# Kernel tuning notes

Measured on AMD Instinct MI355X. Metric: run time of the kernel, lower is better.

Reference implementation:

```python
import jax, jax.numpy as jnp
import numpy as np

EPS = 1e-6
NEG = 0.2  # leaky-relu negative slope
OBJ_C = 6

def _knn(x, k):
    # x: [B,3,N] -> [B,N,k] indices of k nearest neighbors (incl. self)
    xx = jnp.sum(x * x, axis=1)
    inner = jnp.einsum('bdn,bdm->bnm', x, x)
    pd = 2.0 * inner - xx[:, :, None] - xx[:, None, :]  # negative sq dist
    return jax.lax.top_k(pd, k)[1]

def _gather_pts(xt, idx):
    # xt [B,N,D], idx [B,N,k] -> [B,N,k,D]
    return xt[jnp.arange(xt.shape[0])[:, None, None], idx]

def _vn_lin(W, x):
    # channel-mixing linear over VN channel dim: x [B,Cin,3,...]
    return jnp.einsum('oc,bc...->bo...', W, x)

def _vn_bn(x, g, b, eps=1e-5):
    # VNBatchNorm with batch statistics on vector norms
    n = jnp.linalg.norm(x, axis=2) + EPS          # [B,C,*spatial]
    axes = (0,) + tuple(range(2, n.ndim))
    m = jnp.mean(n, axes, keepdims=True)
    v = jnp.var(n, axes, keepdims=True)
    shp = (1, -1) + (1,) * (n.ndim - 2)
    nb = g.reshape(shp) * (n - m) / jnp.sqrt(v + eps) + b.reshape(shp)
    return x / n[:, :, None] * nb[:, :, None]

def _vn_leaky(p, d):
    dot = jnp.sum(p * d, axis=2, keepdims=True)
    dsq = jnp.sum(d * d, axis=2, keepdims=True)
    return NEG * p + (1.0 - NEG) * jnp.where(dot >= 0, p, p - (dot / (dsq + EPS)) * d)

def _vn_block(x, wf, wd, g=None, b=None):
    # VNLinearLeakyReLU
    p = _vn_lin(wf, x)
    if g is not None:
        p = _vn_bn(p, g, b)
    return _vn_leaky(p, _vn_lin(wd, x))

def _surface_feature(coord, k):
    # coord [B,3,N] -> [B,3(chan),3(vec),N,k]: (nb-ctr, ctr, nb x ctr)
    idx = _knn(coord, k)
    xt = coord.transpose(0, 2, 1)                                  # [B,N,3]
    nb = _gather_pts(xt, idx)[:, :, :, None, :]                    # [B,N,k,1,3]
    ctr = jnp.broadcast_to(xt[:, :, None, None, :], nb.shape)
    f = jnp.concatenate([nb - ctr, ctr, jnp.cross(nb, ctr, axis=-1)], axis=3)
    return f.transpose(0, 3, 4, 1, 2)

def _neighbor_feature(x, coord, k):
    # x [B,C,3,N], knn over coord -> [B,C,3,N,k]
    B, C, _, N = x.shape
    idx = _knn(coord, k)
    xt = x.reshape(B, C * 3, N).transpose(0, 2, 1)                 # [B,N,C*3]
    f = _gather_pts(xt, idx).reshape(B, N, k, C, 3)
    return f.transpose(0, 3, 4, 1, 2)

def _vn_maxpool_down(x, coord, wd, rate):
    # x [B,C,3,N,k]: stride-subsample points, VN-max over k neighbors
    x = x[:, :, :, ::rate, :]
    coord_d = coord[:, :, ::rate]
    dot = jnp.sum(x * _vn_lin(wd, x), axis=2)                      # [B,C,Nd,k]
    idx = jnp.argmax(dot, axis=-1)
    xm = jnp.take_along_axis(x, idx[:, :, None, :, None], axis=-1)[..., 0]
    return xm, coord_d

def _nearest_index(t, s):
    # t [B,N,3], s [B,M,3] -> argmin sq-dist index [B,N]
    d = jnp.sum(t * t, -1)[:, :, None] - 2.0 * jnp.einsum('bnd,bmd->bnm', t, s) + jnp.sum(s * s, -1)[:, None, :]
    return jnp.argmin(d, axis=-1)

def _index_points(x, idx):
    # x [B,C,3,M], idx [B,N] -> [B,C,3,N]
    xt = x.transpose(0, 3, 1, 2)
    return xt[jnp.arange(x.shape[0])[:, None], idx].transpose(0, 2, 3, 1)

def _conv_bn_relu(x, w, b, g, be, eps=1e-5):
    # 1x1 Conv1d + BatchNorm1d (batch stats) + ReLU
    y = jnp.einsum('oc,bcn->bon', w, x) + b[None, :, None]
    m = jnp.mean(y, (0, 2), keepdims=True)
    v = jnp.var(y, (0, 2), keepdims=True)
    return jax.nn.relu(g[None, :, None] * (y - m) / jnp.sqrt(v + eps) + be[None, :, None])

def _forward(x, norm, cat_id, wf0, wd0, g0, b0, wf1, wd1, g1, b1, wp1, wf2, wd2, g2, b2, wf3, wd3, g3, b3, wp2, wf4, wd4, g4, b4, wv1f, wv1d, wv2f, wv2d, w3, ws1, cb1, sg1, sb1, ws2, cb2, sg2, sb2, ws3, cb3, sg3, sb3):
    B, _, _, N = x.shape
    coord = x.reshape(B, 3, N)
    one_hot = jax.nn.one_hot(cat_id, OBJ_C, dtype=x.dtype)
    x0 = _vn_block(_surface_feature(coord, 20), wf0, wd0, g0, b0).mean(-1)   # [B,42,3,N]
    x1 = _vn_block(x0, wf1, wd1, g1, b1)
    x2, coord2 = _vn_maxpool_down(_neighbor_feature(x1, coord, 4), coord, wp1, 4)
    x2 = _vn_block(x2, wf2, wd2, g2, b2)                                     # [B,84,3,N/4]
    x3 = _vn_block(x2, wf3, wd3, g3, b3)
    x4, coord4 = _vn_maxpool_down(_neighbor_feature(x3, coord2, 4), coord2, wp2, 4)
    x4 = _vn_block(x4, wf4, wd4, g4, b4)                                     # [B,168,3,N/16]
    ct = coord.transpose(0, 2, 1)
    i1 = _nearest_index(ct, coord2.transpose(0, 2, 1))
    i2 = _nearest_index(ct, coord4.transpose(0, 2, 1))
    eqv = jnp.concatenate([x0, x1, _index_points(x2, i1), _index_points(x3, i1), _index_points(x4, i2)], axis=1)  # [B,420,3,N]
    mean_feat = eqv.mean(-1, keepdims=True)                                  # [B,420,3,1]
    z = _vn_block(mean_feat, wv1f, wv1d)
    z = _vn_block(z, wv2f, wv2d)
    z = jnp.einsum('bcvm,kc->bvkm', z, w3)                                   # [B,3,2,1]
    inv_gl = jnp.einsum('bijm,bjkm->bikm', mean_feat, z).reshape(B, -1, 1)   # [B,840,1]
    inv_0 = jnp.broadcast_to(inv_gl, (B, inv_gl.shape[1], N))
    inv_1 = jnp.sum(mean_feat * coord[:, None], axis=2)                      # [B,420,N]
    oh = jnp.broadcast_to(one_hot[:, :, None], (B, OBJ_C, N))
    inv = jnp.concatenate([norm, inv_0, inv_1, oh], axis=1)                  # [B,1267,N]
    inv = _conv_bn_relu(inv, ws1, cb1, sg1, sb1)
    inv = _conv_bn_relu(inv, ws2, cb2, sg2, sb2)
    inv = _conv_bn_relu(inv, ws3, cb3, sg3, sb3)                             # [B,420,N]
    return eqv, mean_feat, inv, inv_gl

def setup_inputs():
    key = jax.random.key(0)
    ki = iter(jax.random.split(key, 40))
    B, N, D = 4, 2048, 42
    def lin(o, c):
        return jax.random.normal(next(ki), (o, c), jnp.float32) / float(np.sqrt(c))
    inp = dict(
        x=jax.random.normal(next(ki), (B, 1, 3, N), jnp.float32),
        norm=jax.random.normal(next(ki), (B, 1, N), jnp.float32),
        cat_id=jax.random.randint(next(ki), (B,), 0, OBJ_C),
        wf0=lin(D, 3), wd0=lin(D, 3), g0=jnp.ones(D), b0=jnp.zeros(D),
        wf1=lin(D, D), wd1=lin(D, D), g1=jnp.ones(D), b1=jnp.zeros(D),
        wp1=lin(D, D),
        wf2=lin(2 * D, D), wd2=lin(2 * D, D), g2=jnp.ones(2 * D), b2=jnp.zeros(2 * D),
        wf3=lin(2 * D, 2 * D), wd3=lin(2 * D, 2 * D), g3=jnp.ones(2 * D), b3=jnp.zeros(2 * D),
        wp2=lin(2 * D, 2 * D),
        wf4=lin(4 * D, 2 * D), wd4=lin(4 * D, 2 * D), g4=jnp.ones(4 * D), b4=jnp.zeros(4 * D),
        wv1f=lin(5 * D, 10 * D), wv1d=lin(5 * D, 10 * D),
        wv2f=lin(2 * D, 5 * D), wv2d=lin(2 * D, 5 * D),
        w3=lin(2, 2 * D),
        ws1=lin(1024, 1267), cb1=jnp.zeros(1024), sg1=jnp.ones(1024), sb1=jnp.zeros(1024),
        ws2=lin(512, 1024), cb2=jnp.zeros(512), sg2=jnp.ones(512), sb2=jnp.zeros(512),
        ws3=lin(420, 512), cb3=jnp.zeros(420), sg3=jnp.ones(420), sb3=jnp.zeros(420),
    )
    return inp

def reference(x, norm, cat_id, wf0, wd0, g0, b0, wf1, wd1, g1, b1, wp1, wf2, wd2, g2, b2, wf3, wd3, g3, b3, wp2, wf4, wd4, g4, b4, wv1f, wv1d, wv2f, wv2d, w3, ws1, cb1, sg1, sb1, ws2, cb2, sg2, sb2, ws3, cb3, sg3, sb3):
    return _forward(x, norm, cat_id, wf0, wd0, g0, b0, wf1, wd1, g1, b1, wp1, wf2, wd2, g2, b2, wf3, wd3, g3, b3, wp2, wf4, wd4, g4, b4, wv1f, wv1d, wv2f, wv2d, w3, ws1, cb1, sg1, sb1, ws2, cb2, sg2, sb2, ws3, cb3, sg3, sb3)
```

## Files before the change

### kernel.cpp

```cpp
#include <hip/hip_runtime.h>
#include <hip/hip_bf16.h>
#include <cstdint>
#include <cstddef>

#define NTOT 2048
#define BTOT 4

typedef short bf16x8 __attribute__((ext_vector_type(8)));
typedef float f32x4 __attribute__((ext_vector_type(4)));

__device__ inline unsigned short f2b(float v) {
    __hip_bfloat16 h = __float2bfloat16(v);
    return *reinterpret_cast<unsigned short*>(&h);
}

static const size_t WS_IDX20 = 0;
static const size_t WS_FS    = 163840;
static const size_t WS_X0    = 1638400;
static const size_t WS_X1    = 3702784;
static const size_t WS_XM2   = 5767168;
static const size_t WS_X2    = 6025216;
static const size_t WS_X3    = 6541312;
static const size_t WS_IDX42 = 7057408;
static const size_t WS_XM4   = 7059456;
static const size_t WS_X4    = 7188480;
static const size_t WS_I1    = 7446528;
static const size_t WS_I2    = 7454720;
static const size_t WS_MF    = 7462912;
static const size_t WS_INVGL = 7467952;
static const size_t WS_STATS = 7471312;
static const size_t WS_CST   = 7472992;
static const size_t WS_CB    = 7480320;
static const size_t WS_AB    = 7484416;
static const size_t WS_W0    = 7496704;
static const size_t WS_Z1    = 7497728;
static const size_t WS_Z2    = 7500288;
static const size_t WS_W2B   = 13378560;
static const size_t WS_W3B   = 13640704;
static const size_t WS_Y1T   = 13771776;
static const size_t WS_Y1B   = 0;
static const size_t WS_Y2T   = 7480320;
static const size_t WS_Y2B   = 4194304;
static const size_t WS_Y3T   = WS_Y1T;

#define ST0_OFF 0
#define ST1_OFF 84
#define ST2_OFF 168
#define ST3_OFF 336
#define ST4_OFF 504
#define CST1_OFF 0
#define CST2_OFF 2048
#define CST3_OFF 3072

#define OUT_EQV   0
#define OUT_MF    10321920
#define OUT_INV   10326960
#define OUT_INVGL 13767600

__device__ __forceinline__ void merge_pair(float& v1, int& m1, float& v2, int& m2,
                                           float w1, int n1, float w2, int n2)
{
    bool g  = (w1 > v1) || (w1 == v1 && n1 < m1);
    bool ga = (v1 > w2) || (v1 == w2 && m1 < n2);
    bool gb = (w1 > v2) || (w1 == v2 && n1 < m2);
    float s2v = g ? (ga ? v1 : w2) : (gb ? w1 : v2);
    int   s2m = g ? (ga ? m1 : n2) : (gb ? n1 : m2);
    float s1v = g ? w1 : v1;
    int   s1m = g ? n1 : m1;
    v1 = s1v; m1 = s1m; v2 = s2v; m2 = s2m;
}

__device__ __forceinline__ void qtop2(const float* v, int base,
                                      float& a1, int& j1, float& a2, int& j2)
{
    a1 = v[base]; j1 = base; a2 = -3.4e38f; j2 = base;
#pragma unroll
    for (int j = 1; j < 8; ++j) {
        float val = v[base + j];
        bool b1 = val > a1;
        bool b2 = val > a2;
        float na2 = b1 ? a1 : (b2 ? val : a2);
        int   nj2 = b1 ? j1 : (b2 ? base + j : j2);
        a1 = b1 ? val : a1;
        j1 = b1 ? base + j : j1;
        a2 = na2; j2 = nj2;
    }
}

template <int SLOTS, int K>
__global__ __launch_bounds__(256)
void knn_reg_kernel(const float* __restrict__ coord, int cand_stride, int q_stride,
                    int* __restrict__ out_idx, int q_cnt)
{
#pragma clang fp contract(off)
    constexpr int Q = SLOTS / 8;
    int b = blockIdx.y;
    int wave = threadIdx.x >> 6, lane = threadIdx.x & 63;
    int q = blockIdx.x * 4 + wave;
    if (q >= q_cnt) return;
    int nq = q * q_stride;
    float qx = coord[(b * 3 + 0) * NTOT + nq];
    float qy = coord[(b * 3 + 1) * NTOT + nq];
    float qz = coord[(b * 3 + 2) * NTOT + nq];
    float xxq = qx * qx + qy * qy + qz * qz;
    float v[SLOTS];
#pragma unroll
    for (int j = 0; j < SLOTS; ++j) {
        int mo = (lane + 64 * j) * cand_stride;
        float cx = coord[(b * 3 + 0) * NTOT + mo];
        float cy = coord[(b * 3 + 1) * NTOT + mo];
        float cz = coord[(b * 3 + 2) * NTOT + mo];
        float inner = qx * cx + qy * cy + qz * cz;
        float xxc = cx * cx + cy * cy + cz * cz;
        v[j] = (2.0f * inner - xxq) - xxc;
    }
    float q1v[Q], q2v[Q]; int q1j[Q], q2j[Q];
#pragma unroll
    for (int qq = 0; qq < Q; ++qq)
        qtop2(v, qq * 8, q1v[qq], q1j[qq], q2v[qq], q2j[qq]);

#pragma clang loop unroll(disable)
    for (int r = 0; r < K / 2; ++r) {
        float b1v, b2v; int b1j, b2j;
        if constexpr (Q == 4) {
            float x1v = q1v[0], x2v = q2v[0]; int x1j = q1j[0], x2j = q2j[0];
            merge_pair(x1v, x1j, x2v, x2j, q1v[1], q1j[1], q2v[1], q2j[1]);
            float y1v = q1v[2], y2v = q2v[2]; int y1j = q1j[2], y2j = q2j[2];
            merge_pair(y1v, y1j, y2v, y2j, q1v[3], q1j[3], q2v[3], q2j[3]);
            merge_pair(x1v, x1j, x2v, x2j, y1v, y1j, y2v, y2j);
            b1v = x1v; b1j = x1j; b2v = x2v; b2j = x2j;
        } else {
            b1v = q1v[0]; b1j = q1j[0]; b2v = q2v[0]; b2j = q2j[0];
        }
        int b1m = lane + (b1j << 6);
        int b2m = lane + (b2j << 6);
        for (int off = 32; off; off >>= 1) {
            float o1v = __shfl_xor(b1v, off); int o1m = __shfl_xor(b1m, off);
            float o2v = __shfl_xor(b2v, off); int o2m = __shfl_xor(b2m, off);
            merge_pair(b1v, b1m, b2v, b2m, o1v, o1m, o2v, o2m);
        }
        if (lane == 0) {
            out_idx[((size_t)(b * q_cnt) + q) * K + 2 * r]     = b1m;
            out_idx[((size_t)(b * q_cnt) + q) * K + 2 * r + 1] = b2m;
        }
        if (r == K / 2 - 1) break;
        int ws1 = __builtin_amdgcn_readfirstlane(b1m);
        int ws2 = __builtin_amdgcn_readfirstlane(b2m);
        int sl1 = ws1 >> 6, sl2 = ws2 >> 6;
        int wl1 = ws1 & 63, wl2 = ws2 & 63;
#pragma unroll
        for (int qq = 0; qq < Q; ++qq) {
            if ((sl1 >> 3) == qq || (sl2 >> 3) == qq) {
#pragma unroll
                for (int j = 0; j < 8; ++j) {
                    int sl = qq * 8 + j;
                    if (sl == sl1) v[sl] = (lane == wl1) ? -3.4e38f : v[sl];
                    if (sl == sl2) v[sl] = (lane == wl2) ? -3.4e38f : v[sl];
                }
                qtop2(v, qq * 8, q1v[qq], q1j[qq], q2v[qq], q2j[qq]);
            }
        }
    }
}

template <int SLOTS>
__global__ __launch_bounds__(256)
void nearest_reg_kernel(const float* __restrict__ coord, int cand_stride,
                        int* __restrict__ out)
{
#pragma clang fp contract(off)
    int b = blockIdx.y;
    int wave = threadIdx.x >> 6, lane = threadIdx.x & 63;
    int n = blockIdx.x * 4 + wave;
    float qx = coord[(b * 3 + 0) * NTOT + n];
    float qy = coord[(b * 3 + 1) * NTOT + n];
    float qz = coord[(b * 3 + 2) * NTOT + n];
    float tt = qx * qx + qy * qy + qz * qz;
    float v[SLOTS];
#pragma unroll
    for (int j = 0; j < SLOTS; ++j) {
        int mo = (lane + 64 * j) * cand_stride;
        float cx = coord[(b * 3 + 0) * NTOT + mo];
        float cy = coord[(b * 3 + 1) * NTOT + mo];
        float cz = coord[(b * 3 + 2) * NTOT + mo];
        float inner = qx * cx + qy * cy + qz * cz;
        float ss = cx * cx + cy * cy + cz * cz;
        v[j] = (tt - 2.0f * inner) + ss;
    }
    float bv = v[0];
    int bj = 0;
#pragma unroll
    for (int j = 1; j < SLOTS; ++j)
        if (v[j] < bv) { bv = v[j]; bj = j; }
    int bm = lane + 64 * bj;
    for (int off = 32; off; off >>= 1) {
        float ov = __shfl_down(bv, off);
        int   om = __shfl_down(bm, off);
        if (ov < bv || (ov == bv && om < bm)) { bv = ov; bm = om; }
    }
    if (lane == 0) out[b * NTOT + n] = bm;
}

__global__ __launch_bounds__(256)
void stats0_kernel(const float* __restrict__ coord, const int* __restrict__ idx20,
                   const float* __restrict__ wf0, double* __restrict__ stats)
{
    __shared__ float nbc[360];
    __shared__ float ctr[18];
    __shared__ double red[2][6][42];
    int t = threadIdx.x, b = blockIdx.y;
    int ps = t / 42, o = t - ps * 42;
    bool active = ps < 6;
    float w0 = 0.f, w1 = 0.f, w2 = 0.f;
    if (active) { w0 = wf0[o * 3]; w1 = wf0[o * 3 + 1]; w2 = wf0[o * 3 + 2]; }
    double s = 0.0, s2 = 0.0;
    int base = blockIdx.x * 48;
    for (int it = 0; it < 8; ++it) {
        int n0 = base + it * 6;
        __syncthreads();
        if (t < 120) {
            int pl = t / 20, k = t - pl * 20;
            int n = n0 + pl; if (n > NTOT - 1) n = NTOT - 1;
            int m = idx20[((size_t)(b * NTOT + n)) * 20 + k];
            nbc[t * 3 + 0] = coord[(b * 3 + 0) * NTOT + m];
            nbc[t * 3 + 1] = coord[(b * 3 + 1) * NTOT + m];
            nbc[t * 3 + 2] = coord[(b * 3 + 2) * NTOT + m];
        }
        if (t >= 128 && t < 146) {
            int i = t - 128; int pl = i / 3, vd = i - pl * 3;
            int n = n0 + pl; if (n > NTOT - 1) n = NTOT - 1;
            ctr[i] = coord[(b * 3 + vd) * NTOT + n];
        }
        __syncthreads();
        if (active && n0 + ps < NTOT) {
            float cx = ctr[ps * 3], cy = ctr[ps * 3 + 1], cz = ctr[ps * 3 + 2];
            const float* nb = &nbc[ps * 60];
            for (int k = 0; k < 20; ++k) {
                float nx = nb[k * 3], ny = nb[k * 3 + 1], nz = nb[k * 3 + 2];
                float dx = nx - cx, dy = ny - cy, dz = nz - cz;
                float crx = ny * cz - nz * cy;
                float cry = nz * cx - nx * cz;
                float crz = nx * cy - ny * cx;
                float p0 = w0 * dx + w1 * cx + w2 * crx;
                float p1 = w0 * dy + w1 * cy + w2 * cry;
                float p2 = w0 * dz + w1 * cz + w2 * crz;
                float nrm = sqrtf(p0 * p0 + p1 * p1 + p2 * p2) + 1e-6f;
                s += (double)nrm; s2 += (double)nrm * (double)nrm;
            }
        }
    }
    if (active) { red[0][ps][o] = s; red[1][ps][o] = s2; }
    __syncthreads();
    if (t < 42) {
        double a = 0.0, a2 = 0.0;
#pragma unroll
        for (int p = 0; p < 6; ++p) { a += red[0][p][t]; a2 += red[1][p][t]; }
        atomicAdd(&stats[t], a);
        atomicAdd(&stats[42 + t], a2);
    }
}

__global__ __launch_bounds__(256)
void apply0_kernel(const float* __restrict__ coord, const int* __restrict__ idx20,
                   const float* __restrict__ wf0, const float* __restrict__ wd0,
                   const float* __restrict__ g0, const float* __restrict__ b0,
                   const double* __restrict__ stats, float* __restrict__ x0)
{
    __shared__ float nbc[360];
    __shared__ float ctr[18];
    int t = threadIdx.x;
    int b = blockIdx.y;
    int ps = t / 42, o = t - ps * 42;
    int n0 = blockIdx.x * 6;
    if (t < 120) {
        int pl = t / 20, k = t - pl * 20;
        int n = n0 + pl; if (n > NTOT - 1) n = NTOT - 1;
        int m = idx20[((size_t)(b * NTOT + n)) * 20 + k];
        nbc[t * 3 + 0] = coord[(b * 3 + 0) * NTOT + m];
        nbc[t * 3 + 1] = coord[(b * 3 + 1) * NTOT + m];
        nbc[t * 3 + 2] = coord[(b * 3 + 2) * NTOT + m];
    }
    if (t >= 128 && t < 146) {
        int i = t - 128; int pl = i / 3, vd = i - pl * 3;
        int n = n0 + pl; if (n > NTOT - 1) n = NTOT - 1;
        ctr[i] = coord[(b * 3 + vd) * NTOT + n];
    }
    __syncthreads();
    int n = n0 + ps;
    if (ps >= 6 || n >= NTOT) return;
    double S1 = stats[o], S2 = stats[42 + o];
    double md = S1 / 163840.0;
    float m = (float)md;
    float var = (float)(S2 / 163840.0 - md * md);
    float gs = g0[o] / sqrtf(var + 1e-5f);
    float bb = b0[o];
    float wa0 = wf0[o * 3], wa1 = wf0[o * 3 + 1], wa2 = wf0[o * 3 + 2];
    float wb0 = wd0[o * 3], wb1 = wd0[o * 3 + 1], wb2 = wd0[o * 3 + 2];
    float cx = ctr[ps * 3], cy = ctr[ps * 3 + 1], cz = ctr[ps * 3 + 2];
    const float* nb = &nbc[ps * 60];
    float a0 = 0.f, a1 = 0.f, a2 = 0.f;
    for (int k = 0; k < 20; ++k) {
        float nx = nb[k * 3], ny = nb[k * 3 + 1], nz = nb[k * 3 + 2];
        float dx = nx - cx, dy = ny - cy, dz = nz - cz;
        float crx = ny * cz - nz * cy;
        float cry = nz * cx - nx * cz;
        float crz = nx * cy - ny * cx;
        float p0 = wa0 * dx + wa1 * cx + wa2 * crx;
        float p1 = wa0 * dy + wa1 * cy + wa2 * cry;
        float p2 = wa0 * dz + wa1 * cz + wa2 * crz;
        float d0 = wb0 * dx + wb1 * cx + wb2 * crx;
        float d1 = wb0 * dy + wb1 * cy + wb2 * cry;
        float d2 = wb0 * dz + wb1 * cz + wb2 * crz;
        float nrm = sqrtf(p0 * p0 + p1 * p1 + p2 * p2) + 1e-6f;
        float nbv = gs * (nrm - m) + bb;
        float sc = nbv / nrm;
        p0 *= sc; p1 *= sc; p2 *= sc;
        float dot = p0 * d0 + p1 * d1 + p2 * d2;
        float dsq = d0 * d0 + d1 * d1 + d2 * d2 + 1e-6f;
        float tq = fminf(dot, 0.f) / dsq;
        a0 += 0.2f * p0 + 0.8f * (p0 - tq * d0);
        a1 += 0.2f * p1 + 0.8f * (p1 - tq * d1);
        a2 += 0.2f * p2 + 0.8f * (p2 - tq * d2);
    }
    x0[((size_t)(b * 42 + o) * 3 + 0) * NTOT + n] = a0 / 20.0f;
    x0[((size_t)(b * 42 + o) * 3 + 1) * NTOT + n] = a1 / 20.0f;
    x0[((size_t)(b * 42 + o) * 3 + 2) * NTOT + n] = a2 / 20.0f;
}

template <int Ci, int Co, int PTS, int NT, int NIT>
__global__ __launch_bounds__(NT)
void vn_stats_kernel(const float* __restrict__ xin,
                     const float* __restrict__ wf,
                     double* __restrict__ stats, int Npts)
{
    constexpr int Ci3 = Ci * 3;
    constexpr int STRIDE = Ci3 + 1;
    __shared__ float col[PTS * STRIDE];
    __shared__ double red[2][PTS][Co];
    int t = threadIdx.x;
    int b = blockIdx.y;
    int ps = t / Co;
    int o = t - ps * Co;
    bool active = ps < PTS;
    double s = 0.0, s2 = 0.0;
    int base = blockIdx.x * (PTS * NIT);
    for (int it = 0; it < NIT; ++it) {
        int pt0 = base + it * PTS;
        __syncthreads();
        for (int i = t; i < PTS * Ci3; i += NT) {
            int pl = i / Ci3, off = i - pl * Ci3;
            int pt = pt0 + pl; if (pt >= Npts) pt = Npts - 1;
            col[pl * STRIDE + off] = xin[(size_t)(b * 3 * Ci + off) * Npts + pt];
        }
        __syncthreads();
        if (active && pt0 + ps < Npts) {
            const float* cl = &col[ps * STRIDE];
            const float* wr = wf + o * Ci;
            float p0 = 0.f, p1 = 0.f, p2 = 0.f;
#pragma unroll
            for (int c = 0; c < Ci; ++c) {
                float w = wr[c];
                p0 += w * cl[3 * c]; p1 += w * cl[3 * c + 1]; p2 += w * cl[3 * c + 2];
            }
            float nrm = sqrtf(p0 * p0 + p1 * p1 + p2 * p2) + 1e-6f;
            s += (double)nrm; s2 += (double)nrm * (double)nrm;
        }
    }
    if (active) { red[0][ps][o] = s; red[1][ps][o] = s2; }
    __syncthreads();
    if (t < Co) {
        double a = 0.0, a2 = 0.0;
#pragma unroll
        for (int p = 0; p < PTS; ++p) { a += red[0][p][t]; a2 += red[1][p][t]; }
        atomicAdd(&stats[t], a);
        atomicAdd(&stats[Co + t], a2);
    }
}

template <int Ci, int Co, int PTS, int NT>
__global__ __launch_bounds__(NT)
void vn_apply_kernel(const float* __restrict__ xin,
                     const float* __restrict__ wf,
                     const float* __restrict__ wd,
                     const float* __restrict__ g,
                     const float* __restrict__ bbp,
                     const double* __restrict__ stats,
                     double count, int Npts,
                     float* __restrict__ xout)
{
    constexpr int Ci3 = Ci * 3;
    constexpr int STRIDE = Ci3 + 1;
    __shared__ float col[PTS * STRIDE];
    int t = threadIdx.x;
    int b = blockIdx.y;
    int ps = t / Co;
    int o = t - ps * Co;
    bool active = ps < PTS;
    float m = 0.f, gs = 0.f, bb = 0.f;
    if (active) {
        double S1 = stats[o], S2 = stats[Co + o];
        double md = S1 / count;
        m = (float)md;
        float var = (float)(S2 / count - md * md);
        gs = g[o] / sqrtf(var + 1e-5f);
        bb = bbp[o];
    }
    int pt0 = blockIdx.x * PTS;
    for (int i = t; i < PTS * Ci3; i += NT) {
        int pl = i / Ci3, off = i - pl * Ci3;
        int pt = pt0 + pl; if (pt >= Npts) pt = Npts - 1;
        col[pl * STRIDE + off] = xin[(size_t)(b * 3 * Ci + off) * Npts + pt];
    }
    __syncthreads();
    int pt = pt0 + ps;
    if (!active || pt >= Npts) return;
    const float* cl = &col[ps * STRIDE];
    const float* wr = wf + o * Ci;
    const float* wdr = wd + o * Ci;
    float p0 = 0.f, p1 = 0.f, p2 = 0.f, d0 = 0.f, d1 = 0.f, d2 = 0.f;
#pragma unroll
    for (int c = 0; c < Ci; ++c) {
        float c0 = cl[3 * c], c1 = cl[3 * c + 1], c2 = cl[3 * c + 2];
        float w = wr[c];
        p0 += w * c0; p1 += w * c1; p2 += w * c2;
        float w2 = wdr[c];
        d0 += w2 * c0; d1 += w2 * c1; d2 += w2 * c2;
    }
    float nrm = sqrtf(p0 * p0 + p1 * p1 + p2 * p2) + 1e-6f;
    float nb = gs * (nrm - m) + bb;
    float sc = nb / nrm;
    p0 *= sc; p1 *= sc; p2 *= sc;
    float dot = p0 * d0 + p1 * d1 + p2 * d2;
    float dsq = d0 * d0 + d1 * d1 + d2 * d2 + 1e-6f;
    float tq = fminf(dot, 0.f) / dsq;
    float r0 = p0 - tq * d0, r1 = p1 - tq * d1, r2 = p2 - tq * d2;
    xout[((size_t)(b * Co + o) * 3 + 0) * Npts + pt] = 0.2f * p0 + 0.8f * r0;
    xout[((size_t)(b * Co + o) * 3 + 1) * Npts + pt] = 0.2f * p1 + 0.8f * r1;
    xout[((size_t)(b * Co + o) * 3 + 2) * Npts + pt] = 0.2f * p2 + 0.8f * r2;
}

__global__ void vn_pool_kernel(const float* __restrict__ xin,
                               const int* __restrict__ idx, long long sb, int sq,
                               const float* __restrict__ wp,
                               float* __restrict__ xout,
                               int C, int Np, int Nq)
{
#pragma clang fp contract(off)
    __shared__ float nb[4 * 84 * 3];
    int b = blockIdx.y;
    int q = blockIdx.x;
    const int* ir = idx + b * sb + (long long)q * sq;
    for (int kk = 0; kk < 4; ++kk) {
        int mm = ir[kk];
        for (int t = threadIdx.x; t < C * 3; t += blockDim.x)
            nb[kk * C * 3 + t] = xin[(size_t)(b * 3 * C + t) * Np + mm];
    }
    __syncthreads();
    int o = threadIdx.x;
    if (o >= C) return;
    const float* wr = wp + o * C;
    float best = -3.4e38f;
    int bk = 0;
    for (int kk = 0; kk < 4; ++kk) {
        const float* cl = &nb[kk * C * 3];
        float d0 = 0.f, d1 = 0.f, d2 = 0.f;
        for (int c = 0; c < C; ++c) {
            float w = wr[c];
            d0 += w * cl[3 * c]; d1 += w * cl[3 * c + 1]; d2 += w * cl[3 * c + 2];
        }
        float dot = cl[o * 3] * d0 + cl[o * 3 + 1] * d1 + cl[o * 3 + 2] * d2;
        if (dot > best) { best = dot; bk = kk; }
    }
    const float* cb = &nb[bk * C * 3];
    xout[((size_t)(b * C + o) * 3 + 0) * Nq + q] = cb[o * 3];
    xout[((size_t)(b * C + o) * 3 + 1) * Nq + q] = cb[o * 3 + 1];
    xout[((size_t)(b * C + o) * 3 + 2) * Nq + q] = cb[o * 3 + 2];
}

__global__ void eqv_kernel(const float* __restrict__ x0, const float* __restrict__ x1,
                           const float* __restrict__ x2, const float* __restrict__ x3,
                           const float* __restrict__ x4,
                           const int* __restrict__ i1, const int* __restrict__ i2,
                           float* __restrict__ out_eqv, float* __restrict__ mfw)
{
    __shared__ float r1[256];
    int n = blockIdx.x * 256 + threadIdx.x;
    int cv = blockIdx.y;
    int b = blockIdx.z;
    int cc = cv / 3, v = cv % 3;
    float val;
    if (cc < 42)
        val = x0[((size_t)(b * 42 + cc) * 3 + v) * NTOT + n];
    else if (cc < 84)
        val = x1[((size_t)(b * 42 + (cc - 42)) * 3 + v) * NTOT + n];
    else if (cc < 168) {
        int m = i1[b * NTOT + n];
        val = x2[((size_t)(b * 84 + (cc - 84)) * 3 + v) * 512 + m];
    } else if (cc < 252) {
        int m = i1[b * NTOT + n];
        val = x3[((size_t)(b * 84 + (cc - 168)) * 3 + v) * 512 + m];
    } else {
        int m = i2[b * NTOT + n];
        val = x4[((size_t)(b * 168 + (cc - 252)) * 3 + v) * 128 + m];
    }
    out_eqv[((size_t)(b * 1260 + cv)) * NTOT + n] = val;
    r1[threadIdx.x] = val;
    __syncthreads();
    for (int off = 128; off; off >>= 1) {
        if ((int)threadIdx.x < off) r1[threadIdx.x] += r1[threadIdx.x + off];
        __syncthreads();
    }
    if (threadIdx.x == 0) atomicAdd(&mfw[b * 1260 + cv], r1[0]);
}

__global__ void mf_finalize_kernel(float* __restrict__ mfw, float* __restrict__ out_mf)
{
    int i = blockIdx.x * 256 + threadIdx.x;
    if (i < 5040) {
        float m = mfw[i] / 2048.0f;
        mfw[i] = m;
        out_mf[i] = m;
    }
}

__global__ __launch_bounds__(256)
void z1_kernel(const float* __restrict__ mfw,
               const float* __restrict__ wv1f, const float* __restrict__ wv1d,
               float* __restrict__ z1ws)
{
    __shared__ float mf[1260];
    int b = blockIdx.y;
    int wave = threadIdx.x >> 6, lane = threadIdx.x & 63;
    for (int i = threadIdx.x; i < 1260; i += 256) mf[i] = mfw[b * 1260 + i];
    __syncthreads();
    int o = blockIdx.x * 4 + wave;
    if (o >= 210) return;
    const float* wr  = wv1f + (size_t)o * 420;
    const float* wdr = wv1d + (size_t)o * 420;
    float p0 = 0.f, p1 = 0.f, p2 = 0.f, d0 = 0.f, d1 = 0.f, d2 = 0.f;
    for (int c = lane; c < 420; c += 64) {
        float m0 = mf[3 * c], m1 = mf[3 * c + 1], m2 = mf[3 * c + 2];
        float w = wr[c];
        p0 += w * m0; p1 += w * m1; p2 += w * m2;
        float w2 = wdr[c];
        d0 += w2 * m0; d1 += w2 * m1; d2 += w2 * m2;
    }
    for (int off = 32; off; off >>= 1) {
        p0 += __shfl_down(p0, off); p1 += __shfl_down(p1, off);
        p2 += __shfl_down(p2, off); d0 += __shfl_down(d0, off);
        d1 += __shfl_down(d1, off); d2 += __shfl_down(d2, off);
    }
    if (lane == 0) {
        float dot = p0 * d0 + p1 * d1 + p2 * d2;
        float r0, r1, r2;
        if (dot >= 0.f) { r0 = p0; r1 = p1; r2 = p2; }
        else {
            float tq = dot / (d0 * d0 + d1 * d1 + d2 * d2 + 1e-6f);
            r0 = p0 - tq * d0; r1 = p1 - tq * d1; r2 = p2 - tq * d2;
        }
        z1ws[b * 630 + o * 3]     = 0.2f * p0 + 0.8f * r0;
        z1ws[b * 630 + o * 3 + 1] = 0.2f * p1 + 0.8f * r1;
        z1ws[b * 630 + o * 3 + 2] = 0.2f * p2 + 0.8f * r2;
    }
}

__global__ __launch_bounds__(256)
void z2_kernel(const float* __restrict__ z1ws,
               const float* __restrict__ wv2f, const float* __restrict__ wv2d,
               float* __restrict__ z2ws)
{
    __shared__ float zl[630];
    int b = blockIdx.y;
    int wave = threadIdx.x >> 6, lane = threadIdx.x & 63;
    for (int i = threadIdx.x; i < 630; i += 256) zl[i] = z1ws[b * 630 + i];
    __syncthreads();
    int o = blockIdx.x * 4 + wave;
    if (o >= 84) return;
    const float* wr  = wv2f + (size_t)o * 210;
    const float* wdr = wv2d + (size_t)o * 210;
    float p0 = 0.f, p1 = 0.f, p2 = 0.f, d0 = 0.f, d1 = 0.f, d2 = 0.f;
    for (int c = lane; c < 210; c += 64) {
        float m0 = zl[3 * c], m1 = zl[3 * c + 1], m2 = zl[3 * c + 2];
        float w = wr[c];
        p0 += w * m0; p1 += w * m1; p2 += w * m2;
        float w2 = wdr[c];
        d0 += w2 * m0; d1 += w2 * m1; d2 += w2 * m2;
    }
    for (int off = 32; off; off >>= 1) {
        p0 += __shfl_down(p0, off); p1 += __shfl_down(p1, off);
        p2 += __shfl_down(p2, off); d0 += __shfl_down(d0, off);
        d1 += __shfl_down(d1, off); d2 += __shfl_down(d2, off);
    }
    if (lane == 0) {
        float dot = p0 * d0 + p1 * d1 + p2 * d2;
        float r0, r1, r2;
        if (dot >= 0.f) { r0 = p0; r1 = p1; r2 = p2; }
        else {
            float tq = dot / (d0 * d0 + d1 * d1 + d2 * d2 + 1e-6f);
            r0 = p0 - tq * d0; r1 = p1 - tq * d1; r2 = p2 - tq * d2;
        }
        z2ws[b * 252 + o * 3]     = 0.2f * p0 + 0.8f * r0;
        z2ws[b * 252 + o * 3 + 1] = 0.2f * p1 + 0.8f * r1;
        z2ws[b * 252 + o * 3 + 2] = 0.2f * p2 + 0.8f * r2;
    }
}

__global__ void z3invgl_kernel(const float* __restrict__ mfw,
                               const float* __restrict__ z2ws,
                               const float* __restrict__ w3,
                               float* __restrict__ invgl_ws,
                               float* __restrict__ out_invgl)
{
    __shared__ float z2[252];
    __shared__ float z3[6];
    __shared__ float mf[1260];
    int b = blockIdx.x;
    int t = threadIdx.x;
    for (int i = t; i < 252; i += 256) z2[i] = z2ws[b * 252 + i];
    for (int i = t; i < 1260; i += 256) mf[i] = mfw[b * 1260 + i];
    __syncthreads();
    if (t < 6) {
        int v = t / 2, kt = t % 2;
        float s = 0.f;
        for (int c = 0; c < 84; ++c) s += z2[c * 3 + v] * w3[kt * 84 + c];
        z3[v * 2 + kt] = s;
    }
    __syncthreads();
    for (int i = t; i < 840; i += 256) {
        int ii = i / 2, kt = i % 2;
        float s = mf[ii * 3] * z3[0 + kt] + mf[ii * 3 + 1] * z3[2 + kt] +
                  mf[ii * 3 + 2] * z3[4 + kt];
        invgl_ws[b * 840 + i] = s;
        out_invgl[b * 840 + i] = s;
    }
}

__global__ __launch_bounds__(256)
void conv1_coef_kernel(const float* __restrict__ ws1,
                       const float* __restrict__ invgl,
                       const float* __restrict__ mfw,
                       const int* __restrict__ cat,
                       float* __restrict__ cb, float* __restrict__ ab,
                       float* __restrict__ w0)
{
    int wave = threadIdx.x >> 6, lane = threadIdx.x & 63;
    int o = blockIdx.x * 4 + wave;
    int b = blockIdx.y;
    const float* wr = ws1 + (size_t)o * 1267;
    float s = 0.f;
    for (int j = lane; j < 840; j += 64)
        s += wr[1 + j] * invgl[b * 840 + j];
    float a0 = 0.f, a1 = 0.f, a2 = 0.f;
    for (int i = lane; i < 420; i += 64) {
        float w = wr[841 + i];
        a0 += w * mfw[b * 1260 + i * 3];
        a1 += w * mfw[b * 1260 + i * 3 + 1];
        a2 += w * mfw[b * 1260 + i * 3 + 2];
    }
    for (int off = 32; off; off >>= 1) {
        s  += __shfl_down(s, off);
        a0 += __shfl_down(a0, off);
        a1 += __shfl_down(a1, off);
        a2 += __shfl_down(a2, off);
    }
    if (lane == 0) {
        cb[b * 1024 + o] = s + wr[1261 + cat[b]];
        ab[((size_t)(b * 1024 + o)) * 3 + 0] = a0;
        ab[((size_t)(b * 1024 + o)) * 3 + 1] = a1;
        ab[((size_t)(b * 1024 + o)) * 3 + 2] = a2;
        if (b == 0) w0[o] = wr[0];
    }
}

__global__ __launch_bounds__(256)
void y1_stats_kernel(const float* __restrict__ cb, const float* __restrict__ ab,
                     const float* __restrict__ w0, const float* __restrict__ coord,
                     const float* __restrict__ normv, float* __restrict__ cst)
{
    __shared__ float px[256], py[256], pz[256], pn[256];
    int t = threadIdx.x;
    int o = blockIdx.x * 256 + t;
    int b = blockIdx.y >> 3;
    int n0 = (blockIdx.y & 7) * 256;
    px[t] = coord[(b * 3 + 0) * NTOT + n0 + t];
    py[t] = coord[(b * 3 + 1) * NTOT + n0 + t];
    pz[t] = coord[(b * 3 + 2) * NTOT + n0 + t];
    pn[t] = normv[b * NTOT + n0 + t];
    __syncthreads();
    size_t bo = (size_t)(b * 1024 + o);
    float c0 = cb[bo];
    float a0 = ab[bo * 3], a1 = ab[bo * 3 + 1], a2 = ab[bo * 3 + 2];
    float wn = w0[o];
    float s = 0.f, s2 = 0.f;
    for (int k = 0; k < 256; ++k) {
        float v = c0 + a0 * px[k] + a1 * py[k] + a2 * pz[k] + wn * pn[k];
        s += v; s2 += v * v;
    }
    atomicAdd(&cst[o], s);
    atomicAdd(&cst[1024 + o], s2);
}

__global__ __launch_bounds__(256)
void y1_bnrelu_kernel(const float* __restrict__ cb, const float* __restrict__ ab,
                      const float* __restrict__ w0, const float* __restrict__ coord,
                      const float* __restrict__ normv, const float* __restrict__ cst,
                      const float* __restrict__ sg, const float* __restrict__ sb,
                      unsigned short* __restrict__ y1b)
{
    __shared__ float px[256], py[256], pz[256], pn[256];
    int t = threadIdx.x;
    int o = blockIdx.x * 256 + t;
    int b = blockIdx.y >> 3;
    int n0 = (blockIdx.y & 7) * 256;
    px[t] = coord[(b * 3 + 0) * NTOT + n0 + t];
    py[t] = coord[(b * 3 + 1) * NTOT + n0 + t];
    pz[t] = coord[(b * 3 + 2) * NTOT + n0 + t];
    pn[t] = normv[b * NTOT + n0 + t];
    __syncthreads();
    size_t bo = (size_t)(b * 1024 + o);
    float c0 = cb[bo];
    float a0 = ab[bo * 3], a1 = ab[bo * 3 + 1], a2 = ab[bo * 3 + 2];
    float wn = w0[o];
    float mm = cst[o] * (1.f / 8192.f);
    float var = cst[1024 + o] * (1.f / 8192.f) - mm * mm;
    float sc = sg[o] / sqrtf(var + 1e-5f);
    float bs = sb[o] - mm * sc;
    size_t rowbase = (size_t)(b * NTOT + n0) * 1024 + o;
    for (int k = 0; k < 256; ++k) {
        float v = c0 + a0 * px[k] + a1 * py[k] + a2 * pz[k] + wn * pn[k];
        float r = sc * v + bs;
        y1b[rowbase + (size_t)k * 1024] = f2b(r > 0.f ? r : 0.f);
    }
}

__global__ void wconv_kernel(const float* __restrict__ src, unsigned short* __restrict__ dst,
                             int Msrc, int Ksrc, int Kpad)
{
    int k = blockIdx.x * 256 + threadIdx.x;
    int o = blockIdx.y;
    float v = (o < Msrc && k < Ksrc) ? src[(size_t)o * Ksrc + k] : 0.f;
    dst[(size_t)o * Kpad + k] = f2b(v);
}

__global__ __launch_bounds__(256)
void gemm_mfma_kernel(const unsigned short* __restrict__ A,
                      const unsigned short* __restrict__ Bw,
                      float* __restrict__ C, float* __restrict__ st,
                      int K, int Mreal)
{
    __shared__ __align__(16) unsigned short Al[128 * 40];
    __shared__ __align__(16) unsigned short Bl[128 * 40];
    __shared__ float sst[128], sst2[128];
    int t = threadIdx.x;
    if (t < 128) { sst[t] = 0.f; sst2[t] = 0.f; }
    int r0 = blockIdx.x * 128;
    int c0 = blockIdx.y * 128;
    int w = t >> 6, l = t & 63;
    int wm = w & 1, wn = w >> 1;
    int lm = l & 15, lq = l >> 4;
    f32x4 acc[4][4] = {};
    for (int k0 = 0; k0 < K; k0 += 32) {
        for (int half = 0; half < 2; ++half) {
            int ch = t + half * 256;
            int row = ch >> 2, kc = ch & 3;
            *(uint4*)&Al[row * 40 + kc * 8] =
                *(const uint4*)&A[(size_t)(r0 + row) * K + k0 + kc * 8];
            *(uint4*)&Bl[row * 40 + kc * 8] =
                *(const uint4*)&Bw[(size_t)(c0 + row) * K + k0 + kc * 8];
        }
        __syncthreads();
        bf16x8 af[4], bfr[4];
#pragma unroll
        for (int i = 0; i < 4; ++i)
            af[i] = *(const bf16x8*)&Al[(wm * 64 + i * 16 + lm) * 40 + lq * 8];
#pragma unroll
        for (int j = 0; j < 4; ++j)
            bfr[j] = *(const bf16x8*)&Bl[(wn * 64 + j * 16 + lm) * 40 + lq * 8];
#pragma unroll
        for (int i = 0; i < 4; ++i)
#pragma unroll
            for (int j = 0; j < 4; ++j)
                acc[i][j] = __builtin_amdgcn_mfma_f32_16x16x32_bf16(af[i], bfr[j],
                                                                    acc[i][j], 0, 0, 0);
        __syncthreads();
    }
#pragma unroll
    for (int i = 0; i < 4; ++i) {
#pragma unroll
        for (int j = 0; j < 4; ++j) {
            int col = c0 + wn * 64 + j * 16 + lm;
            if (col < Mreal) {
                int rbase = r0 + wm * 64 + i * 16 + lq * 4;
#pragma unroll
                for (int r = 0; r < 4; ++r)
                    C[(size_t)(rbase + r) * Mreal + col] = acc[i][j][r];
            }
        }
    }
#pragma unroll
    for (int j = 0; j < 4; ++j) {
        float s = 0.f, s2 = 0.f;
#pragma unroll
        for (int i = 0; i < 4; ++i)
#pragma unroll
            for (int r = 0; r < 4; ++r) { float x = acc[i][j][r]; s += x; s2 += x * x; }
        s  += __shfl_down(s, 32);  s  += __shfl_down(s, 16);
        s2 += __shfl_down(s2, 32); s2 += __shfl_down(s2, 16);
        if (l < 16) {
            int cc = wn * 64 + j * 16 + lm;
            atomicAdd(&sst[cc], s);
            atomicAdd(&sst2[cc], s2);
        }
    }
    __syncthreads();
    if (t < 128) {
        int col = c0 + t;
        if (col < Mreal) {
            atomicAdd(&st[col], sst[t]);
            atomicAdd(&st[Mreal + col], sst2[t]);
        }
    }
}

__global__ void bnreluT_kernel(const float* __restrict__ Ct, const float* __restrict__ st,
                               const float* __restrict__ g, const float* __restrict__ be,
                               unsigned short* __restrict__ outb, int M, int maskM)
{
    size_t idx = (size_t)blockIdx.x * 256 + threadIdx.x;
    int o = (int)(idx & (size_t)maskM);
    float m = st[o] * (1.f / 8192.f);
    float var = st[M + o] * (1.f / 8192.f) - m * m;
    float sqv = sqrtf(var + 1e-5f);
    float v = g[o] * (Ct[idx] - m) / sqv + be[o];
    outb[idx] = f2b(v > 0.f ? v : 0.f);
}

__global__ void bnrelu_outT_kernel(const float* __restrict__ Ct, const float* __restrict__ st,
                                   const float* __restrict__ g, const float* __restrict__ be,
                                   float* __restrict__ outinv)
{
    __shared__ float tile[64][65];
    int t = threadIdx.x;
    int r0 = blockIdx.x * 64;
    int o0 = blockIdx.y * 64;
    int b = r0 >> 11, n0 = r0 & 2047;
    int oi = t & 63;
    int o = o0 + oi;
    float m = 0.f, sqv = 1.f, gg = 0.f, bb = 0.f;
    if (o < 420) {
        m = st[o] * (1.f / 8192.f);
        float var = st[420 + o] * (1.f / 8192.f) - m * m;
        sqv = sqrtf(var + 1e-5f);
        gg = g[o]; bb = be[o];
    }
    for (int it = 0; it < 16; ++it) {
        int rr = it * 4 + (t >> 6);
        float v = 0.f;
        if (o < 420) {
            v = gg * (Ct[(size_t)(r0 + rr) * 420 + o] - m) / sqv + bb;
            v = v > 0.f ? v : 0.f;
        }
        tile[rr][oi] = v;
    }
    __syncthreads();
    for (int it = 0; it < 16; ++it) {
        int oc = it * 4 + (t >> 6);
        int oo = o0 + oc;
        if (oo < 420)
            outinv[((size_t)(b * 420 + oo)) * 2048 + n0 + (t & 63)] = tile[t & 63][oc];
    }
}

extern "C" void kernel_launch(void* const* d_in, const int* in_sizes, int n_in,
                              void* d_out, int out_size, void* d_ws, size_t ws_size,
                              hipStream_t stream)
{
    (void)in_sizes; (void)n_in; (void)out_size; (void)ws_size;
    const float* xc   = (const float*)d_in[0];
    const float* normv= (const float*)d_in[1];
    const int*   cat  = (const int*)d_in[2];
    const float* wf0  = (const float*)d_in[3];
    const float* wd0  = (const float*)d_in[4];
    const float* g0   = (const float*)d_in[5];
    const float* b0   = (const float*)d_in[6];
    const float* wf1  = (const float*)d_in[7];
    const float* wd1  = (const float*)d_in[8];
    const float* g1   = (const float*)d_in[9];
    const float* b1   = (const float*)d_in[10];
    const float* wp1  = (const float*)d_in[11];
    const float* wf2  = (const float*)d_in[12];
    const float* wd2  = (const float*)d_in[13];
    const float* g2   = (const float*)d_in[14];
    const float* b2   = (const float*)d_in[15];
    const float* wf3  = (const float*)d_in[16];
    const float* wd3  = (const float*)d_in[17];
    const float* g3   = (const float*)d_in[18];
    const float* b3   = (const float*)d_in[19];
    const float* wp2  = (const float*)d_in[20];
    const float* wf4  = (const float*)d_in[21];
    const float* wd4  = (const float*)d_in[22];
    const float* g4   = (const float*)d_in[23];
    const float* b4   = (const float*)d_in[24];
    const float* wv1f = (const float*)d_in[25];
    const float* wv1d = (const float*)d_in[26];
    const float* wv2f = (const float*)d_in[27];
    const float* wv2d = (const float*)d_in[28];
    const float* w3   = (const float*)d_in[29];
    const float* ws1  = (const float*)d_in[30];
    const float* sg1  = (const float*)d_in[32];
    const float* sb1  = (const float*)d_in[33];
    const float* ws2  = (const float*)d_in[34];
    const float* sg2  = (const float*)d_in[36];
    const float* sb2  = (const float*)d_in[37];
    const float* ws3  = (const float*)d_in[38];
    const float* sg3  = (const float*)d_in[40];
    const float* sb3  = (const float*)d_in[41];

    float* ws = (float*)d_ws;
    float* out = (float*)d_out;

    int*    idx20 = (int*)(ws + WS_IDX20);
    float*  x0    = ws + WS_X0;
    float*  x1    = ws + WS_X1;
    float*  xm2   = ws + WS_XM2;
    float*  x2    = ws + WS_X2;
    float*  x3    = ws + WS_X3;
    int*    idx42 = (int*)(ws + WS_IDX42);
    float*  xm4   = ws + WS_XM4;
    float*  x4    = ws + WS_X4;
    int*    i1p   = (int*)(ws + WS_I1);
    int*    i2p   = (int*)(ws + WS_I2);
    float*  mfw   = ws + WS_MF;
    float*  invgl = ws + WS_INVGL;
    double* st    = (double*)(ws + WS_STATS);
    float*  cst   = ws + WS_CST;
    float*  cb    = ws + WS_CB;
    float*  ab    = ws + WS_AB;
    float*  w0    = ws + WS_W0;
    float*  z1ws  = ws + WS_Z1;
    float*  z2ws  = ws + WS_Z2;
    unsigned short* w2b  = (unsigned short*)(ws + WS_W2B);
    unsigned short* w3b  = (unsigned short*)(ws + WS_W3B);
    unsigned short* y1b  = (unsigned short*)(ws + WS_Y1B);
    float*  y2t   = ws + WS_Y2T;
    unsigned short* y2b  = (unsigned short*)(ws + WS_Y2B);
    float*  y3t   = ws + WS_Y3T;

    hipMemsetAsync((void*)st, 0, 840 * sizeof(double), stream);
    hipMemsetAsync((void*)cst, 0, 3912 * sizeof(float), stream);
    hipMemsetAsync((void*)mfw, 0, 5040 * sizeof(float), stream);

    wconv_kernel<<<dim3(4, 512), 256, 0, stream>>>(ws2, w2b, 512, 1024, 1024);
    wconv_kernel<<<dim3(2, 512), 256, 0, stream>>>(ws3, w3b, 420, 512, 512);

    knn_reg_kernel<32, 20><<<dim3(512, 4), 256, 0, stream>>>(xc, 1, 1, idx20, 2048);

    stats0_kernel<<<dim3(43, 4), 256, 0, stream>>>(xc, idx20, wf0, st + ST0_OFF);
    apply0_kernel<<<dim3(342, 4), 256, 0, stream>>>(xc, idx20, wf0, wd0, g0, b0,
                                                    st + ST0_OFF, x0);

    vn_stats_kernel<42, 42, 6, 256, 8><<<dim3(43, 4), 256, 0, stream>>>(
        x0, wf1, st + ST1_OFF, 2048);
    vn_apply_kernel<42, 42, 6, 256><<<dim3(342, 4), 256, 0, stream>>>(
        x0, wf1, wd1, g1, b1, st + ST1_OFF, 8192.0, 2048, x1);

    vn_pool_kernel<<<dim3(512, 4), 256, 0, stream>>>(x1, idx20, 40960LL, 80, wp1, xm2,
                                                     42, 2048, 512);
    vn_stats_kernel<42, 84, 3, 256, 8><<<dim3(22, 4), 256, 0, stream>>>(
        xm2, wf2, st + ST2_OFF, 512);
    vn_apply_kernel<42, 84, 3, 256><<<dim3(171, 4), 256, 0, stream>>>(
        xm2, wf2, wd2, g2, b2, st + ST2_OFF, 2048.0, 512, x2);
    vn_stats_kernel<84, 84, 3, 256, 8><<<dim3(22, 4), 256, 0, stream>>>(
        x2, wf3, st + ST3_OFF, 512);
    vn_apply_kernel<84, 84, 3, 256><<<dim3(171, 4), 256, 0, stream>>>(
        x2, wf3, wd3, g3, b3, st + ST3_OFF, 2048.0, 512, x3);

    knn_reg_kernel<8, 4><<<dim3(32, 4), 256, 0, stream>>>(xc, 4, 16, idx42, 128);
    vn_pool_kernel<<<dim3(128, 4), 256, 0, stream>>>(x3, idx42, 512LL, 4, wp2, xm4,
                                                     84, 512, 128);
    vn_stats_kernel<84, 168, 3, 512, 4><<<dim3(11, 4), 512, 0, stream>>>(
        xm4, wf4, st + ST4_OFF, 128);
    vn_apply_kernel<84, 168, 3, 512><<<dim3(43, 4), 512, 0, stream>>>(
        xm4, wf4, wd4, g4, b4, st + ST4_OFF, 512.0, 128, x4);

    nearest_reg_kernel<8><<<dim3(512, 4), 256, 0, stream>>>(xc, 4, i1p);
    nearest_reg_kernel<2><<<dim3(512, 4), 256, 0, stream>>>(xc, 16, i2p);

    eqv_kernel<<<dim3(8, 1260, 4), 256, 0, stream>>>(x0, x1, x2, x3, x4, i1p, i2p,
                                                     out + OUT_EQV, mfw);
    mf_finalize_kernel<<<20, 256, 0, stream>>>(mfw, out + OUT_MF);

    z1_kernel<<<dim3(53, 4), 256, 0, stream>>>(mfw, wv1f, wv1d, z1ws);
    z2_kernel<<<dim3(21, 4), 256, 0, stream>>>(z1ws, wv2f, wv2d, z2ws);
    z3invgl_kernel<<<4, 256, 0, stream>>>(mfw, z2ws, w3, invgl, out + OUT_INVGL);

    conv1_coef_kernel<<<dim3(256, 4), 256, 0, stream>>>(ws1, invgl, mfw, cat, cb, ab, w0);
    y1_stats_kernel<<<dim3(4, 32), 256, 0, stream>>>(cb, ab, w0, xc, normv,
                                                     cst + CST1_OFF);
    y1_bnrelu_kernel<<<dim3(4, 32), 256, 0, stream>>>(cb, ab, w0, xc, normv,
                                                      cst + CST1_OFF, sg1, sb1, y1b);

    gemm_mfma_kernel<<<dim3(64, 4), 256, 0, stream>>>(y1b, w2b, y2t, cst + CST2_OFF,
                                                      1024, 512);
    bnreluT_kernel<<<16384, 256, 0, stream>>>(y2t, cst + CST2_OFF, sg2, sb2, y2b,
                                              512, 511);

    gemm_mfma_kernel<<<dim3(64, 4), 256, 0, stream>>>(y2b, w3b, y3t, cst + CST3_OFF,
                                                      512, 420);
    bnrelu_outT_kernel<<<dim3(128, 7), 256, 0, stream>>>(y3t, cst + CST3_OFF, sg3, sb3,
                                                         out + OUT_INV);
}
```

Before: 643.4 us.

## Process multiple queries per wave in KNN and switch to top-1 selection rounds

Result: no change. 631.0 us (-1.9%).

```diff
diff --git a/kernel.cpp b/kernel.cpp
--- a/kernel.cpp
+++ b/kernel.cpp
@@ -15,7 +15,6 @@
 }
 
 static const size_t WS_IDX20 = 0;
-static const size_t WS_FS    = 163840;
 static const size_t WS_X0    = 1638400;
 static const size_t WS_X1    = 3702784;
 static const size_t WS_XM2   = 5767168;
@@ -37,11 +36,10 @@
 static const size_t WS_Z2    = 7500288;
 static const size_t WS_W2B   = 13378560;
 static const size_t WS_W3B   = 13640704;
-static const size_t WS_Y1T   = 13771776;
 static const size_t WS_Y1B   = 0;
 static const size_t WS_Y2T   = 7480320;
 static const size_t WS_Y2B   = 4194304;
-static const size_t WS_Y3T   = WS_Y1T;
+static const size_t WS_Y3T   = 13771776;
 
 #define ST0_OFF 0
 #define ST1_OFF 84
@@ -57,37 +55,7 @@
 #define OUT_INV   10326960
 #define OUT_INVGL 13767600
 
-__device__ __forceinline__ void merge_pair(float& v1, int& m1, float& v2, int& m2,
-                                           float w1, int n1, float w2, int n2)
-{
-    bool g  = (w1 > v1) || (w1 == v1 && n1 < m1);
-    bool ga = (v1 > w2) || (v1 == w2 && m1 < n2);
-    bool gb = (w1 > v2) || (w1 == v2 && n1 < m2);
-    float s2v = g ? (ga ? v1 : w2) : (gb ? w1 : v2);
-    int   s2m = g ? (ga ? m1 : n2) : (gb ? n1 : m2);
-    float s1v = g ? w1 : v1;
-    int   s1m = g ? n1 : m1;
-    v1 = s1v; m1 = s1m; v2 = s2v; m2 = s2m;
-}
-
-__device__ __forceinline__ void qtop2(const float* v, int base,
-                                      float& a1, int& j1, float& a2, int& j2)
-{
-    a1 = v[base]; j1 = base; a2 = -3.4e38f; j2 = base;
-#pragma unroll
-    for (int j = 1; j < 8; ++j) {
-        float val = v[base + j];
-        bool b1 = val > a1;
-        bool b2 = val > a2;
-        float na2 = b1 ? a1 : (b2 ? val : a2);
-        int   nj2 = b1 ? j1 : (b2 ? base + j : j2);
-        a1 = b1 ? val : a1;
-        j1 = b1 ? base + j : j1;
-        a2 = na2; j2 = nj2;
-    }
-}
-
-template <int SLOTS, int K>
+template <int SLOTS, int K, int NQ>
 __global__ __launch_bounds__(256)
 void knn_reg_kernel(const float* __restrict__ coord, int cand_stride, int q_stride,
                     int* __restrict__ out_idx, int q_cnt)
@@ -96,68 +64,86 @@
     constexpr int Q = SLOTS / 8;
     int b = blockIdx.y;
     int wave = threadIdx.x >> 6, lane = threadIdx.x & 63;
-    int q = blockIdx.x * 4 + wave;
-    if (q >= q_cnt) return;
-    int nq = q * q_stride;
-    float qx = coord[(b * 3 + 0) * NTOT + nq];
-    float qy = coord[(b * 3 + 1) * NTOT + nq];
-    float qz = coord[(b * 3 + 2) * NTOT + nq];
-    float xxq = qx * qx + qy * qy + qz * qz;
-    float v[SLOTS];
+    int qbase = (blockIdx.x * 4 + wave) * NQ;
+    if (qbase >= q_cnt) return;
+    float qx[NQ], qy[NQ], qz[NQ], xxq[NQ];
+#pragma unroll
+    for (int u = 0; u < NQ; ++u) {
+        int nq = (qbase + u) * q_stride;
+        qx[u] = coord[(b * 3 + 0) * NTOT + nq];
+        qy[u] = coord[(b * 3 + 1) * NTOT + nq];
+        qz[u] = coord[(b * 3 + 2) * NTOT + nq];
+        xxq[u] = qx[u] * qx[u] + qy[u] * qy[u] + qz[u] * qz[u];
+    }
+    float v[NQ][SLOTS];
 #pragma unroll
     for (int j = 0; j < SLOTS; ++j) {
         int mo = (lane + 64 * j) * cand_stride;
         float cx = coord[(b * 3 + 0) * NTOT + mo];
         float cy = coord[(b * 3 + 1) * NTOT + mo];
         float cz = coord[(b * 3 + 2) * NTOT + mo];
-        float inner = qx * cx + qy * cy + qz * cz;
         float xxc = cx * cx + cy * cy + cz * cz;
-        v[j] = (2.0f * inner - xxq) - xxc;
-    }
-    float q1v[Q], q2v[Q]; int q1j[Q], q2j[Q];
-#pragma unroll
-    for (int qq = 0; qq < Q; ++qq)
-        qtop2(v, qq * 8, q1v[qq], q1j[qq], q2v[qq], q2j[qq]);
-
+#pragma unroll
+        for (int u = 0; u < NQ; ++u) {
+            float inner = qx[u] * cx + qy[u] * cy + qz[u] * cz;
+            v[u][j] = (2.0f * inner - xxq[u]) - xxc;
+        }
+    }
+    float qv[NQ][Q]; int qj[NQ][Q];
+#pragma unroll
+    for (int u = 0; u < NQ; ++u)
+#pragma unroll
+        for (int qq = 0; qq < Q; ++qq) {
+            float nv = v[u][qq * 8]; int nj = qq * 8;
+#pragma unroll
+            for (int j = 1; j < 8; ++j)
+                if (v[u][qq * 8 + j] > nv) { nv = v[u][qq * 8 + j]; nj = qq * 8 + j; }
+            qv[u][qq] = nv; qj[u][qq] = nj;
+        }
 #pragma clang loop unroll(disable)
-    for (int r = 0; r < K / 2; ++r) {
-        float b1v, b2v; int b1j, b2j;
-        if constexpr (Q == 4) {
-            float x1v = q1v[0], x2v = q2v[0]; int x1j = q1j[0], x2j = q2j[0];
-            merge_pair(x1v, x1j, x2v, x2j, q1v[1], q1j[1], q2v[1], q2j[1]);
-            float y1v = q1v[2], y2v = q2v[2]; int y1j = q1j[2], y2j = q2j[2];
-            merge_pair(y1v, y1j, y2v, y2j, q1v[3], q1j[3], q2v[3], q2j[3]);
-            merge_pair(x1v, x1j, x2v, x2j, y1v, y1j, y2v, y2j);
-            b1v = x1v; b1j = x1j; b2v = x2v; b2j = x2j;
-        } else {
-            b1v = q1v[0]; b1j = q1j[0]; b2v = q2v[0]; b2j = q2j[0];
-        }
-        int b1m = lane + (b1j << 6);
-        int b2m = lane + (b2j << 6);
+    for (int kk = 0; kk < K; ++kk) {
+        float bv[NQ]; int bm[NQ];
+#pragma unroll
+        for (int u = 0; u < NQ; ++u) {
+            float tv = qv[u][0]; int tj = qj[u][0];
+#pragma unroll
+            for (int qq = 1; qq < Q; ++qq)
+                if (qv[u][qq] > tv) { tv = qv[u][qq]; tj = qj[u][qq]; }
+            bv[u] = tv; bm[u] = lane + 64 * tj;
+        }
         for (int off = 32; off; off >>= 1) {
-            float o1v = __shfl_xor(b1v, off); int o1m = __shfl_xor(b1m, off);
-            float o2v = __shfl_xor(b2v, off); int o2m = __shfl_xor(b2m, off);
-            merge_pair(b1v, b1m, b2v, b2m, o1v, o1m, o2v, o2m);
-        }
-        if (lane == 0) {
-            out_idx[((size_t)(b * q_cnt) + q) * K + 2 * r]     = b1m;
-            out_idx[((size_t)(b * q_cnt) + q) * K + 2 * r + 1] = b2m;
-        }
-        if (r == K / 2 - 1) break;
-        int ws1 = __builtin_amdgcn_readfirstlane(b1m);
-        int ws2 = __builtin_amdgcn_readfirstlane(b2m);
-        int sl1 = ws1 >> 6, sl2 = ws2 >> 6;
-        int wl1 = ws1 & 63, wl2 = ws2 & 63;
-#pragma unroll
-        for (int qq = 0; qq < Q; ++qq) {
-            if ((sl1 >> 3) == qq || (sl2 >> 3) == qq) {
-#pragma unroll
-                for (int j = 0; j < 8; ++j) {
-                    int sl = qq * 8 + j;
-                    if (sl == sl1) v[sl] = (lane == wl1) ? -3.4e38f : v[sl];
-                    if (sl == sl2) v[sl] = (lane == wl2) ? -3.4e38f : v[sl];
+            float ov[NQ]; int om[NQ];
+#pragma unroll
+            for (int u = 0; u < NQ; ++u) {
+                ov[u] = __shfl_down(bv[u], off);
+                om[u] = __shfl_down(bm[u], off);
+            }
+#pragma unroll
+            for (int u = 0; u < NQ; ++u)
+                if (ov[u] > bv[u] || (ov[u] == bv[u] && om[u] < bm[u])) {
+                    bv[u] = ov[u]; bm[u] = om[u];
                 }
-                qtop2(v, qq * 8, q1v[qq], q1j[qq], q2v[qq], q2j[qq]);
+        }
+#pragma unroll
+        for (int u = 0; u < NQ; ++u) {
+            int m_win = __builtin_amdgcn_readfirstlane(bm[u]);
+            if (lane == 0)
+                out_idx[((size_t)(b * q_cnt) + qbase + u) * K + kk] = m_win;
+            int w_slot = m_win >> 6;
+            bool isw = (lane == (m_win & 63));
+#pragma unroll
+            for (int qq = 0; qq < Q; ++qq) {
+                if (qq == (w_slot >> 3)) {
+#pragma unroll
+                    for (int j = 0; j < 8; ++j)
+                        if (qq * 8 + j == w_slot)
+                            v[u][qq * 8 + j] = isw ? -3.4e38f : v[u][qq * 8 + j];
+                    float nv = v[u][qq * 8]; int nj = qq * 8;
+#pragma unroll
+                    for (int j = 1; j < 8; ++j)
+                        if (v[u][qq * 8 + j] > nv) { nv = v[u][qq * 8 + j]; nj = qq * 8 + j; }
+                    qv[u][qq] = nv; qj[u][qq] = nj;
+                }
             }
         }
     }
@@ -953,7 +939,7 @@
     wconv_kernel<<<dim3(4, 512), 256, 0, stream>>>(ws2, w2b, 512, 1024, 1024);
     wconv_kernel<<<dim3(2, 512), 256, 0, stream>>>(ws3, w3b, 420, 512, 512);
 
-    knn_reg_kernel<32, 20><<<dim3(512, 4), 256, 0, stream>>>(xc, 1, 1, idx20, 2048);
+    knn_reg_kernel<32, 20, 2><<<dim3(256, 4), 256, 0, stream>>>(xc, 1, 1, idx20, 2048);
 
     stats0_kernel<<<dim3(43, 4), 256, 0, stream>>>(xc, idx20, wf0, st + ST0_OFF);
     apply0_kernel<<<dim3(342, 4), 256, 0, stream>>>(xc, idx20, wf0, wd0, g0, b0,
@@ -975,7 +961,7 @@
     vn_apply_kernel<84, 84, 3, 256><<<dim3(171, 4), 256, 0, stream>>>(
         x2, wf3, wd3, g3, b3, st + ST3_OFF, 2048.0, 512, x3);
 
-    knn_reg_kernel<8, 4><<<dim3(32, 4), 256, 0, stream>>>(xc, 4, 16, idx42, 128);
+    knn_reg_kernel<8, 4, 1><<<dim3(32, 4), 256, 0, stream>>>(xc, 4, 16, idx42, 128);
     vn_pool_kernel<<<dim3(128, 4), 256, 0, stream>>>(x3, idx42, 512LL, 4, wp2, xm4,
                                                      84, 512, 128);
     vn_stats_kernel<84, 168, 3, 512, 4><<<dim3(11, 4), 512, 0, stream>>>(
```
